# Optimization experiments

Measured on AMD Instinct MI355X. Metric: run time of the kernel, lower is better.

## Reference

```python
import jax, jax.numpy as jnp
import numpy as np

N_NODES = 100000
N_EDGES = 1600000
IN_CH, HID_CH, OUT_CH = 256, 128, 64


def setup_inputs() -> dict:
    key = jax.random.key(0)
    k_x, k_e, k1, k2, kb1, kb2 = jax.random.split(key, 6)
    x = jax.random.normal(k_x, (N_NODES, IN_CH), dtype=jnp.float32)
    edge_index = jax.random.randint(k_e, (2, N_EDGES), 0, N_NODES, dtype=jnp.int64)
    # Glorot-style init for GCN linear weights
    W1 = jax.random.normal(k1, (IN_CH, HID_CH), dtype=jnp.float32) * (1.0 / np.sqrt(IN_CH))
    b1 = jnp.zeros((HID_CH,), dtype=jnp.float32)
    W2 = jax.random.normal(k2, (HID_CH, OUT_CH), dtype=jnp.float32) * (1.0 / np.sqrt(HID_CH))
    b2 = jnp.zeros((OUT_CH,), dtype=jnp.float32)
    return {"x": x, "edge_index": edge_index, "W1": W1, "b1": b1, "W2": W2, "b2": b2}


def _gcn_norm(edge_index, n_nodes):
    # add self loops, compute D^{-1/2} (A+I) D^{-1/2} edge weights (PyG gcn_norm)
    loop = jnp.arange(n_nodes, dtype=edge_index.dtype)
    src = jnp.concatenate([edge_index[0], loop])
    dst = jnp.concatenate([edge_index[1], loop])
    deg = jax.ops.segment_sum(jnp.ones_like(src, dtype=jnp.float32), dst, num_segments=n_nodes)
    dinv = jnp.where(deg > 0, jax.lax.rsqrt(jnp.maximum(deg, 1.0)), 0.0)
    norm = dinv[src] * dinv[dst]  # [E + N]
    return src, dst, norm


def _gcn_conv(x, W, b, src, dst, norm, n_nodes):
    h = x @ W                         # linear first (PyG GCNConv)
    msg = norm[:, None] * h[src]      # gather + normalize  [E+N, out]
    agg = jax.ops.segment_sum(msg, dst, num_segments=n_nodes)
    return agg + b


def reference(x, edge_index, W1, b1, W2, b2):
    n = x.shape[0]
    src, dst, norm = _gcn_norm(edge_index, n)
    h = jax.nn.relu(_gcn_conv(x, W1, b1, src, dst, norm, n))
    # dropout is identity in eval mode
    z = _gcn_conv(h, W2, b2, src, dst, norm, n)
    # inner-product decoder on the provided edges, with sigmoid
    e_src, e_dst = edge_index[0], edge_index[1]
    logits = jnp.sum(z[e_src] * z[e_dst], axis=-1)
    return jax.nn.sigmoid(logits)
```

## Files before the change

### kernel.cpp

```cpp
#include <hip/hip_runtime.h>
#include <math.h>

#define N_NODES 100000
#define N_EDGES 1600000
#define IN_CH 256
#define HID_CH 128
#define OUT_CH 64
#define NTILES ((N_NODES + 63) / 64)
#define NB 1024
#define NPART 256
#define EPB (N_EDGES / NPART)
#define NB_USED ((N_NODES + 127) / 128)

typedef short s16x8 __attribute__((ext_vector_type(8)));
typedef unsigned short u16x8 __attribute__((ext_vector_type(8)));
typedef float f32x4 __attribute__((ext_vector_type(4)));

__device__ __forceinline__ float bf2f(unsigned short u) {
    union { unsigned int i; float f; } v;
    v.i = ((unsigned int)u) << 16;
    return v.f;
}
__device__ __forceinline__ unsigned short f2bf(float f) {
    union { float f; unsigned int i; } v;
    v.f = f;
    unsigned int u = v.i;
    return (unsigned short)((u + 0x7FFFu + ((u >> 16) & 1u)) >> 16);
}


__global__ __launch_bounds__(256) void k_hist(const int* __restrict__ dst,
                                              int* __restrict__ ghist) {
    __shared__ int h[NB];
    int b = blockIdx.x, t = threadIdx.x;
    for (int k = t; k < NB; k += 256) h[k] = 0;
    __syncthreads();
    int e0 = b * EPB;
    for (int e = e0 + t; e < e0 + EPB; e += 256)
        atomicAdd(&h[dst[e] >> 7], 1);
    __syncthreads();
    for (int k = t; k < NB; k += 256) ghist[k * NPART + b] = h[k];
}

__global__ __launch_bounds__(256) void k_scan_cols(const int* __restrict__ ghist,
                                                   int* __restrict__ goff,
                                                   int* __restrict__ btot) {
    __shared__ int tmp[NPART];
    int k = blockIdx.x, t = threadIdx.x;
    int v = ghist[k * NPART + t];
    tmp[t] = v;
    __syncthreads();
    for (int off = 1; off < NPART; off <<= 1) {
        int u = (t >= off) ? tmp[t - off] : 0;
        __syncthreads();
        tmp[t] += u;
        __syncthreads();
    }
    goff[k * NPART + t] = tmp[t] - v;
    if (t == NPART - 1) btot[k] = tmp[t];
}

__global__ __launch_bounds__(1024) void k_scan_base(const int* __restrict__ btot,
                                                    int* __restrict__ bbase) {
    __shared__ int tmp[NB];
    int t = threadIdx.x;
    int v = btot[t];
    tmp[t] = v;
    __syncthreads();
    for (int off = 1; off < NB; off <<= 1) {
        int u = (t >= off) ? tmp[t - off] : 0;
        __syncthreads();
        tmp[t] += u;
        __syncthreads();
    }
    bbase[t] = tmp[t] - v;
    if (t == NB - 1) bbase[NB] = tmp[t];
}

__global__ __launch_bounds__(256) void k_partition(const int* __restrict__ src,
                                                   const int* __restrict__ dst,
                                                   const int* __restrict__ goff,
                                                   const int* __restrict__ bbase,
                                                   int* __restrict__ bsorted_p) {
    __shared__ int cur[NB];
    int b = blockIdx.x, t = threadIdx.x;
    for (int k = t; k < NB; k += 256) cur[k] = bbase[k] + goff[k * NPART + b];
    __syncthreads();
    int e0 = b * EPB;
    for (int e = e0 + t; e < e0 + EPB; e += 256) {
        int s = src[e], d = dst[e];
        int pos = atomicAdd(&cur[d >> 7], 1);
        bsorted_p[pos] = (s << 7) | (d & 127);
    }
}

__global__ __launch_bounds__(256) void k_bucket_csr(const int* __restrict__ bsorted_p,
                                                    const int* __restrict__ bbase,
                                                    int* __restrict__ rowoff,
                                                    float* __restrict__ dinv,
                                                    int* __restrict__ csr_src) {
    __shared__ int cnt[128];
    __shared__ int tmp[256];
    __shared__ int cur[128];
    int b = blockIdx.x, t = threadIdx.x;
    int ebeg = bbase[b], eend = bbase[b + 1];
    if (t < 128) cnt[t] = 0;
    __syncthreads();
    for (int e = ebeg + t; e < eend; e += 256)
        atomicAdd(&cnt[bsorted_p[e] & 127], 1);
    __syncthreads();
    int v = (t < 128) ? cnt[t] : 0;
    tmp[t] = v;
    __syncthreads();
    for (int off = 1; off < 256; off <<= 1) {
        int u = (t >= off) ? tmp[t - off] : 0;
        __syncthreads();
        tmp[t] += u;
        __syncthreads();
    }
    if (t < 128) {
        int base = ebeg + tmp[t] - v;
        cur[t] = base;
        int node = b * 128 + t;
        if (node < N_NODES) {
            rowoff[node] = base;
            dinv[node] = rsqrtf((float)v + 1.0f);
        }
    }
    __syncthreads();
    for (int e = ebeg + t; e < eend; e += 256) {
        int v2 = bsorted_p[e];
        int pos = atomicAdd(&cur[v2 & 127], 1);
        csr_src[pos] = v2 >> 7;
    }
}

__global__ __launch_bounds__(256) void k_cast(const float* __restrict__ x,
                                              unsigned short* __restrict__ xb) {
    const int total = N_NODES * IN_CH / 8;
    int stride = gridDim.x * 256;
    for (int i = blockIdx.x * 256 + threadIdx.x; i < total; i += stride) {
        f32x4 a = *reinterpret_cast<const f32x4*>(x + (size_t)i * 8);
        f32x4 b = *reinterpret_cast<const f32x4*>(x + (size_t)i * 8 + 4);
        u16x8 o;
        o[0] = f2bf(a[0]); o[1] = f2bf(a[1]); o[2] = f2bf(a[2]); o[3] = f2bf(a[3]);
        o[4] = f2bf(b[0]); o[5] = f2bf(b[1]); o[6] = f2bf(b[2]); o[7] = f2bf(b[3]);
        *reinterpret_cast<u16x8*>(xb + (size_t)i * 8) = o;
    }
}

__global__ void k_wt1(const float* __restrict__ W1, unsigned short* __restrict__ Wf1) {
    int u = blockIdx.x * 256 + threadIdx.x;
    int f = u >> 6, lane = u & 63;
    int kk = f >> 3, nt = f & 7;
    int l15 = lane & 15, lhi = lane >> 4;
    int n = nt * 16 + l15;
    int kbase = kk * 32 + lhi * 8;
    #pragma unroll
    for (int j = 0; j < 8; ++j)
        Wf1[(size_t)u * 8 + j] = f2bf(W1[(size_t)(kbase + j) * HID_CH + n]);
}

__global__ void k_wt2(const float* __restrict__ W2, unsigned short* __restrict__ Wf2) {
    int u = blockIdx.x * 256 + threadIdx.x;
    int f = u >> 6, lane = u & 63;
    int kk = f >> 2, nt = f & 3;
    int l15 = lane & 15, lhi = lane >> 4;
    int n = nt * 16 + l15;
    int kbase = kk * 32 + lhi * 8;
    #pragma unroll
    for (int j = 0; j < 8; ++j)
        Wf2[(size_t)u * 8 + j] = f2bf(W2[(size_t)(kbase + j) * OUT_CH + n]);
}

__global__ __launch_bounds__(256, 4) void k_gemm1(const unsigned short* __restrict__ xb,
                                                  const unsigned short* __restrict__ Wf1,
                                                  const float* __restrict__ dinv,
                                                  unsigned short* __restrict__ hs1) {
    int tid = threadIdx.x;
    int w = tid >> 6;
    int lane = tid & 63;
    int l15 = lane & 15;
    int lhi = lane >> 4;
    int m0 = blockIdx.x * 64;

    int arow = m0 + w * 16 + l15;
    int arowc = (arow < N_NODES) ? arow : (N_NODES - 1);
    const s16x8* ap = reinterpret_cast<const s16x8*>(xb + (size_t)arowc * IN_CH) + lhi;

    s16x8 af[8];
    #pragma unroll
    for (int kk = 0; kk < 8; ++kk) af[kk] = ap[kk * 4];

    const s16x8* wp = reinterpret_cast<const s16x8*>(Wf1) + lane;

    f32x4 acc[8] = {};
    #pragma unroll
    for (int kk = 0; kk < 8; ++kk) {
        #pragma unroll
        for (int nt = 0; nt < 8; ++nt) {
            s16x8 bf = wp[(kk * 8 + nt) * 64];
            acc[nt] = __builtin_amdgcn_mfma_f32_16x16x32_bf16(af[kk], bf, acc[nt], 0, 0, 0);
        }
    }

    float dv[4];
    int rb = m0 + w * 16 + lhi * 4;
    #pragma unroll
    for (int r = 0; r < 4; ++r) dv[r] = (rb + r < N_NODES) ? dinv[rb + r] : 0.0f;
    #pragma unroll
    for (int nt = 0; nt < 8; ++nt) {
        #pragma unroll
        for (int r = 0; r < 4; ++r) {
            int row = rb + r;
            if (row < N_NODES)
                hs1[(size_t)row * HID_CH + nt * 16 + l15] = f2bf(dv[r] * acc[nt][r]);
        }
    }
}

__global__ __launch_bounds__(256, 4) void k_gemm2(const unsigned short* __restrict__ h1r,
                                                  const unsigned short* __restrict__ Wf2,
                                                  const float* __restrict__ dinv,
                                                  unsigned short* __restrict__ hs2) {
    int tid = threadIdx.x;
    int w = tid >> 6;
    int lane = tid & 63;
    int l15 = lane & 15;
    int lhi = lane >> 4;
    int m0 = blockIdx.x * 64;

    int arow = m0 + w * 16 + l15;
    int arowc = (arow < N_NODES) ? arow : (N_NODES - 1);
    const s16x8* ap = reinterpret_cast<const s16x8*>(h1r + (size_t)arowc * HID_CH) + lhi;

    s16x8 af[4];
    #pragma unroll
    for (int kk = 0; kk < 4; ++kk) af[kk] = ap[kk * 4];

    const s16x8* wp = reinterpret_cast<const s16x8*>(Wf2) + lane;

    f32x4 acc[4] = {};
    #pragma unroll
    for (int kk = 0; kk < 4; ++kk) {
        #pragma unroll
        for (int nt = 0; nt < 4; ++nt) {
            s16x8 bf = wp[(kk * 4 + nt) * 64];
            acc[nt] = __builtin_amdgcn_mfma_f32_16x16x32_bf16(af[kk], bf, acc[nt], 0, 0, 0);
        }
    }

    float dv[4];
    int rb = m0 + w * 16 + lhi * 4;
    #pragma unroll
    for (int r = 0; r < 4; ++r) dv[r] = (rb + r < N_NODES) ? dinv[rb + r] : 0.0f;
    #pragma unroll
    for (int nt = 0; nt < 4; ++nt) {
        #pragma unroll
        for (int r = 0; r < 4; ++r) {
            int row = rb + r;
            if (row < N_NODES)
                hs2[(size_t)row * OUT_CH + nt * 16 + l15] = f2bf(dv[r] * acc[nt][r]);
        }
    }
}

template <int C, bool RELU>
__global__ __launch_bounds__(256) void k_gather_agg(const int* __restrict__ rowoff,
                                                    const int* __restrict__ csr_src,
                                                    const unsigned short* __restrict__ hs,
                                                    const float* __restrict__ dinv,
                                                    const float* __restrict__ b,
                                                    unsigned short* __restrict__ outp) {
    constexpr int TPN = C / 8;
    constexpr int NPB = 256 / TPN;
    int t = threadIdx.x;
    int node = blockIdx.x * NPB + t / TPN;
    int q = t % TPN;
    if (node >= N_NODES) return;

    int beg = rowoff[node];
    int end = (node + 1 < N_NODES) ? rowoff[node + 1] : N_EDGES;

    float acc[8];
    {
        u16x8 sv = *reinterpret_cast<const u16x8*>(&hs[(size_t)node * C + q * 8]);
        #pragma unroll
        for (int j = 0; j < 8; ++j) acc[j] = bf2f(sv[j]);
    }

    int i = beg;
    for (; i + 3 < end; i += 4) {
        int s0 = csr_src[i], s1 = csr_src[i + 1], s2 = csr_src[i + 2], s3 = csr_src[i + 3];
        u16x8 v0 = *reinterpret_cast<const u16x8*>(&hs[(size_t)s0 * C + q * 8]);
        u16x8 v1 = *reinterpret_cast<const u16x8*>(&hs[(size_t)s1 * C + q * 8]);
        u16x8 v2 = *reinterpret_cast<const u16x8*>(&hs[(size_t)s2 * C + q * 8]);
        u16x8 v3 = *reinterpret_cast<const u16x8*>(&hs[(size_t)s3 * C + q * 8]);
        #pragma unroll
        for (int j = 0; j < 8; ++j)
            acc[j] += (bf2f(v0[j]) + bf2f(v1[j])) + (bf2f(v2[j]) + bf2f(v3[j]));
    }
    for (; i < end; ++i) {
        int s0 = csr_src[i];
        u16x8 v0 = *reinterpret_cast<const u16x8*>(&hs[(size_t)s0 * C + q * 8]);
        #pragma unroll
        for (int j = 0; j < 8; ++j) acc[j] += bf2f(v0[j]);
    }

    float w = dinv[node];
    float4 b0 = reinterpret_cast<const float4*>(b)[q * 2];
    float4 b1 = reinterpret_cast<const float4*>(b)[q * 2 + 1];
    float bb[8] = {b0.x, b0.y, b0.z, b0.w, b1.x, b1.y, b1.z, b1.w};
    u16x8 o;
    #pragma unroll
    for (int j = 0; j < 8; ++j) {
        float v = w * acc[j] + bb[j];
        if (RELU) v = fmaxf(v, 0.0f);
        o[j] = f2bf(v);
    }
    *reinterpret_cast<u16x8*>(&outp[(size_t)node * C + q * 8]) = o;
}


__global__ __launch_bounds__(256) void k_decode(const int* __restrict__ esrc,
                                                const int* __restrict__ edst,
                                                const unsigned short* __restrict__ z,
                                                float* __restrict__ out) {
    int tid = threadIdx.x;
    int e = blockIdx.x * 32 + tid / 8;
    int q = tid % 8;
    if (e >= N_EDGES) return;
    int s = esrc[e], d = edst[e];
    u16x8 a = *reinterpret_cast<const u16x8*>(&z[(size_t)s * OUT_CH + q * 8]);
    u16x8 b = *reinterpret_cast<const u16x8*>(&z[(size_t)d * OUT_CH + q * 8]);
    float dot = 0.0f;
    #pragma unroll
    for (int j = 0; j < 8; ++j) dot += bf2f(a[j]) * bf2f(b[j]);
    dot += __shfl_xor(dot, 1);
    dot += __shfl_xor(dot, 2);
    dot += __shfl_xor(dot, 4);
    if (q == 0) out[e] = 1.0f / (1.0f + expf(-dot));
}


extern "C" void kernel_launch(void* const* d_in, const int* in_sizes, int n_in,
                              void* d_out, int out_size, void* d_ws, size_t ws_size,
                              hipStream_t stream) {
    const float* x  = (const float*)d_in[0];
    const int*   ei = (const int*)d_in[1];
    const float* W1 = (const float*)d_in[2];
    const float* b1 = (const float*)d_in[3];
    const float* W2 = (const float*)d_in[4];
    const float* b2 = (const float*)d_in[5];
    float* out = (float*)d_out;

    const int* src = ei;
    const int* dst = ei + N_EDGES;

    char* ws = (char*)d_ws;
    int*   ghist   = (int*)(ws + 0x000000);
    int*   goff    = (int*)(ws + 0x100000);
    int*   btot    = (int*)(ws + 0x200000);
    int*   bbase   = (int*)(ws + 0x202000);
    int*   rowoff  = (int*)(ws + 0x210000);
    float* dinv    = (float*)(ws + 0x290000);
    unsigned short* Wf1 = (unsigned short*)(ws + 0x310000);
    unsigned short* Wf2 = (unsigned short*)(ws + 0x320000);
    int*   csr_src = (int*)(ws + 0x400000);
    int*   bsorted_p = (int*)(ws + 0xB00000);
    unsigned short* xb  = (unsigned short*)(ws + 0xB00000);
    unsigned short* hs1 = (unsigned short*)(ws + 0x3C00000);
    unsigned short* h1r = (unsigned short*)(ws + 0xB00000);
    unsigned short* hs2 = (unsigned short*)(ws + 0x3C00000);
    unsigned short* z   = (unsigned short*)(ws + 0x2800000);

    k_hist<<<NPART, 256, 0, stream>>>(dst, ghist);
    k_scan_cols<<<NB, 256, 0, stream>>>(ghist, goff, btot);
    k_scan_base<<<1, NB, 0, stream>>>(btot, bbase);
    k_partition<<<NPART, 256, 0, stream>>>(src, dst, goff, bbase, bsorted_p);
    k_bucket_csr<<<NB_USED, 256, 0, stream>>>(bsorted_p, bbase, rowoff, dinv, csr_src);

    k_cast<<<2048, 256, 0, stream>>>(x, xb);
    k_wt1<<<16, 256, 0, stream>>>(W1, Wf1);
    k_wt2<<<4, 256, 0, stream>>>(W2, Wf2);

    k_gemm1<<<NTILES, 256, 0, stream>>>(xb, Wf1, dinv, hs1);
    k_gather_agg<HID_CH, true><<<(N_NODES * 16 + 255) / 256, 256, 0, stream>>>(
        rowoff, csr_src, hs1, dinv, b1, h1r);

    k_gemm2<<<NTILES, 256, 0, stream>>>(h1r, Wf2, dinv, hs2);
    k_gather_agg<OUT_CH, false><<<(N_NODES * 8 + 255) / 256, 256, 0, stream>>>(
        rowoff, csr_src, hs2, dinv, b2, z);

    k_decode<<<N_EDGES / 32, 256, 0, stream>>>(src, dst, z, out);
}
```

Baseline: 254.4 us.

## Fuse preprocessing kernels and overlap GEMM1 with edge partitioning

Merges cast, histogram and weight-swizzle kernels into one launch with role-based block dispatch, and runs the first GEMM in the same launch as the edge partition. To drop GEMM1's dependency on dinv, the source-side degree scaling moves into the first gather, which now multiplies each neighbour row by dinv[src]. Workspace buffers are re-laid out so the overlapping roles do not alias. This cuts launch count and serialization at the cost of extra per-edge dinv loads in the gather.

```diff
diff --git a/kernel.cpp b/kernel.cpp
--- a/kernel.cpp
+++ b/kernel.cpp
@@ -11,6 +11,7 @@
 #define NPART 256
 #define EPB (N_EDGES / NPART)
 #define NB_USED ((N_NODES + 127) / 128)
+#define CAST_BLKS 2048
 
 typedef short s16x8 __attribute__((ext_vector_type(8)));
 typedef unsigned short u16x8 __attribute__((ext_vector_type(8)));
@@ -29,18 +30,64 @@
 }
 
 
-__global__ __launch_bounds__(256) void k_hist(const int* __restrict__ dst,
-                                              int* __restrict__ ghist) {
+__device__ __forceinline__ void role_cast(int b, const float* __restrict__ x,
+                                          unsigned short* __restrict__ xb) {
+    const int total = N_NODES * IN_CH / 8;
+    int stride = CAST_BLKS * 256;
+    for (int i = b * 256 + threadIdx.x; i < total; i += stride) {
+        f32x4 a = *reinterpret_cast<const f32x4*>(x + (size_t)i * 8);
+        f32x4 c = *reinterpret_cast<const f32x4*>(x + (size_t)i * 8 + 4);
+        u16x8 o;
+        o[0] = f2bf(a[0]); o[1] = f2bf(a[1]); o[2] = f2bf(a[2]); o[3] = f2bf(a[3]);
+        o[4] = f2bf(c[0]); o[5] = f2bf(c[1]); o[6] = f2bf(c[2]); o[7] = f2bf(c[3]);
+        *reinterpret_cast<u16x8*>(xb + (size_t)i * 8) = o;
+    }
+}
+
+__global__ __launch_bounds__(256) void k_fused_pre(const float* __restrict__ x,
+                                                   const int* __restrict__ dst,
+                                                   const float* __restrict__ W1,
+                                                   const float* __restrict__ W2,
+                                                   unsigned short* __restrict__ xb,
+                                                   int* __restrict__ ghist,
+                                                   unsigned short* __restrict__ Wf1,
+                                                   unsigned short* __restrict__ Wf2) {
     __shared__ int h[NB];
     int b = blockIdx.x, t = threadIdx.x;
-    for (int k = t; k < NB; k += 256) h[k] = 0;
-    __syncthreads();
-    int e0 = b * EPB;
-    for (int e = e0 + t; e < e0 + EPB; e += 256)
-        atomicAdd(&h[dst[e] >> 7], 1);
-    __syncthreads();
-    for (int k = t; k < NB; k += 256) ghist[k * NPART + b] = h[k];
-}
+    if (b < CAST_BLKS) {
+        role_cast(b, x, xb);
+    } else if (b < CAST_BLKS + NPART) {
+        int hb = b - CAST_BLKS;
+        for (int k = t; k < NB; k += 256) h[k] = 0;
+        __syncthreads();
+        int e0 = hb * EPB;
+        for (int e = e0 + t; e < e0 + EPB; e += 256)
+            atomicAdd(&h[dst[e] >> 7], 1);
+        __syncthreads();
+        for (int k = t; k < NB; k += 256) ghist[k * NPART + hb] = h[k];
+    } else if (b < CAST_BLKS + NPART + 16) {
+        int u = (b - CAST_BLKS - NPART) * 256 + t;
+        int f = u >> 6, lane = u & 63;
+        int kk = f >> 3, nt = f & 7;
+        int l15 = lane & 15, lhi = lane >> 4;
+        int n = nt * 16 + l15;
+        int kbase = kk * 32 + lhi * 8;
+        #pragma unroll
+        for (int j = 0; j < 8; ++j)
+            Wf1[(size_t)u * 8 + j] = f2bf(W1[(size_t)(kbase + j) * HID_CH + n]);
+    } else {
+        int u = (b - CAST_BLKS - NPART - 16) * 256 + t;
+        int f = u >> 6, lane = u & 63;
+        int kk = f >> 2, nt = f & 3;
+        int l15 = lane & 15, lhi = lane >> 4;
+        int n = nt * 16 + l15;
+        int kbase = kk * 32 + lhi * 8;
+        #pragma unroll
+        for (int j = 0; j < 8; ++j)
+            Wf2[(size_t)u * 8 + j] = f2bf(W2[(size_t)(kbase + j) * OUT_CH + n]);
+    }
+}
+
 
 __global__ __launch_bounds__(256) void k_scan_cols(const int* __restrict__ ghist,
                                                    int* __restrict__ goff,
@@ -77,22 +124,67 @@
     if (t == NB - 1) bbase[NB] = tmp[t];
 }
 
-__global__ __launch_bounds__(256) void k_partition(const int* __restrict__ src,
+
+__global__ __launch_bounds__(256) void k_fused_mid(const int* __restrict__ src,
                                                    const int* __restrict__ dst,
                                                    const int* __restrict__ goff,
                                                    const int* __restrict__ bbase,
-                                                   int* __restrict__ bsorted_p) {
+                                                   int* __restrict__ bsorted_p,
+                                                   const unsigned short* __restrict__ xb,
+                                                   const unsigned short* __restrict__ Wf1,
+                                                   unsigned short* __restrict__ h1) {
     __shared__ int cur[NB];
     int b = blockIdx.x, t = threadIdx.x;
-    for (int k = t; k < NB; k += 256) cur[k] = bbase[k] + goff[k * NPART + b];
-    __syncthreads();
-    int e0 = b * EPB;
-    for (int e = e0 + t; e < e0 + EPB; e += 256) {
-        int s = src[e], d = dst[e];
-        int pos = atomicAdd(&cur[d >> 7], 1);
-        bsorted_p[pos] = (s << 7) | (d & 127);
-    }
-}
+    if (b < NPART) {
+        for (int k = t; k < NB; k += 256) cur[k] = bbase[k] + goff[k * NPART + b];
+        __syncthreads();
+        int e0 = b * EPB;
+        for (int e = e0 + t; e < e0 + EPB; e += 256) {
+            int s = src[e], d = dst[e];
+            int pos = atomicAdd(&cur[d >> 7], 1);
+            bsorted_p[pos] = (s << 7) | (d & 127);
+        }
+    } else {
+        int mt = b - NPART;
+        int w = t >> 6;
+        int lane = t & 63;
+        int l15 = lane & 15;
+        int lhi = lane >> 4;
+        int m0 = mt * 64;
+
+        int arow = m0 + w * 16 + l15;
+        int arowc = (arow < N_NODES) ? arow : (N_NODES - 1);
+        const s16x8* ap = reinterpret_cast<const s16x8*>(xb + (size_t)arowc * IN_CH) + lhi;
+
+        s16x8 af[8];
+        #pragma unroll
+        for (int kk = 0; kk < 8; ++kk) af[kk] = ap[kk * 4];
+
+        const s16x8* wp = reinterpret_cast<const s16x8*>(Wf1) + lane;
+
+        f32x4 acc[8] = {};
+        #pragma unroll
+        for (int kk = 0; kk < 8; ++kk) {
+            #pragma unroll
+            for (int nt = 0; nt < 8; ++nt) {
+                s16x8 bf = wp[(kk * 8 + nt) * 64];
+                acc[nt] = __builtin_amdgcn_mfma_f32_16x16x32_bf16(af[kk], bf, acc[nt], 0, 0, 0);
+            }
+        }
+
+        int rb = m0 + w * 16 + lhi * 4;
+        #pragma unroll
+        for (int nt = 0; nt < 8; ++nt) {
+            #pragma unroll
+            for (int r = 0; r < 4; ++r) {
+                int row = rb + r;
+                if (row < N_NODES)
+                    h1[(size_t)row * HID_CH + nt * 16 + l15] = f2bf(acc[nt][r]);
+            }
+        }
+    }
+}
+
 
 __global__ __launch_bounds__(256) void k_bucket_csr(const int* __restrict__ bsorted_p,
                                                     const int* __restrict__ bbase,
@@ -135,88 +227,57 @@
     }
 }
 
-__global__ __launch_bounds__(256) void k_cast(const float* __restrict__ x,
-                                              unsigned short* __restrict__ xb) {
-    const int total = N_NODES * IN_CH / 8;
-    int stride = gridDim.x * 256;
-    for (int i = blockIdx.x * 256 + threadIdx.x; i < total; i += stride) {
-        f32x4 a = *reinterpret_cast<const f32x4*>(x + (size_t)i * 8);
-        f32x4 b = *reinterpret_cast<const f32x4*>(x + (size_t)i * 8 + 4);
-        u16x8 o;
-        o[0] = f2bf(a[0]); o[1] = f2bf(a[1]); o[2] = f2bf(a[2]); o[3] = f2bf(a[3]);
-        o[4] = f2bf(b[0]); o[5] = f2bf(b[1]); o[6] = f2bf(b[2]); o[7] = f2bf(b[3]);
-        *reinterpret_cast<u16x8*>(xb + (size_t)i * 8) = o;
-    }
-}
-
-__global__ void k_wt1(const float* __restrict__ W1, unsigned short* __restrict__ Wf1) {
-    int u = blockIdx.x * 256 + threadIdx.x;
-    int f = u >> 6, lane = u & 63;
-    int kk = f >> 3, nt = f & 7;
-    int l15 = lane & 15, lhi = lane >> 4;
-    int n = nt * 16 + l15;
-    int kbase = kk * 32 + lhi * 8;
+__global__ __launch_bounds__(256) void k_gather1(const int* __restrict__ rowoff,
+                                                 const int* __restrict__ csr_src,
+                                                 const unsigned short* __restrict__ h1,
+                                                 const float* __restrict__ dinv,
+                                                 const float* __restrict__ b,
+                                                 unsigned short* __restrict__ outp) {
+    int t = threadIdx.x;
+    int node = blockIdx.x * 16 + t / 16;
+    int q = t % 16;
+    if (node >= N_NODES) return;
+
+    int beg = rowoff[node];
+    int end = (node + 1 < N_NODES) ? rowoff[node + 1] : N_EDGES;
+    float wd = dinv[node];
+
+    float acc[8];
+    {
+        u16x8 sv = *reinterpret_cast<const u16x8*>(&h1[(size_t)node * HID_CH + q * 8]);
+        #pragma unroll
+        for (int j = 0; j < 8; ++j) acc[j] = wd * bf2f(sv[j]);
+    }
+
+    int i = beg;
+    for (; i + 3 < end; i += 4) {
+        int s0 = csr_src[i], s1 = csr_src[i + 1], s2 = csr_src[i + 2], s3 = csr_src[i + 3];
+        float d0 = dinv[s0], d1 = dinv[s1], d2 = dinv[s2], d3 = dinv[s3];
+        u16x8 v0 = *reinterpret_cast<const u16x8*>(&h1[(size_t)s0 * HID_CH + q * 8]);
+        u16x8 v1 = *reinterpret_cast<const u16x8*>(&h1[(size_t)s1 * HID_CH + q * 8]);
+        u16x8 v2 = *reinterpret_cast<const u16x8*>(&h1[(size_t)s2 * HID_CH + q * 8]);
+        u16x8 v3 = *reinterpret_cast<const u16x8*>(&h1[(size_t)s3 * HID_CH + q * 8]);
+        #pragma unroll
+        for (int j = 0; j < 8; ++j)
+            acc[j] += (d0 * bf2f(v0[j]) + d1 * bf2f(v1[j])) +
+                      (d2 * bf2f(v2[j]) + d3 * bf2f(v3[j]));
+    }
+    for (; i < end; ++i) {
+        int s0 = csr_src[i];
+        float d0 = dinv[s0];
+        u16x8 v0 = *reinterpret_cast<const u16x8*>(&h1[(size_t)s0 * HID_CH + q * 8]);
+        #pragma unroll
+        for (int j = 0; j < 8; ++j) acc[j] += d0 * bf2f(v0[j]);
+    }
+
+    float4 b0 = reinterpret_cast<const float4*>(b)[q * 2];
+    float4 b1 = reinterpret_cast<const float4*>(b)[q * 2 + 1];
+    float bb[8] = {b0.x, b0.y, b0.z, b0.w, b1.x, b1.y, b1.z, b1.w};
+    u16x8 o;
     #pragma unroll
     for (int j = 0; j < 8; ++j)
-        Wf1[(size_t)u * 8 + j] = f2bf(W1[(size_t)(kbase + j) * HID_CH + n]);
-}
-
-__global__ void k_wt2(const float* __restrict__ W2, unsigned short* __restrict__ Wf2) {
-    int u = blockIdx.x * 256 + threadIdx.x;
-    int f = u >> 6, lane = u & 63;
-    int kk = f >> 2, nt = f & 3;
-    int l15 = lane & 15, lhi = lane >> 4;
-    int n = nt * 16 + l15;
-    int kbase = kk * 32 + lhi * 8;
-    #pragma unroll
-    for (int j = 0; j < 8; ++j)
-        Wf2[(size_t)u * 8 + j] = f2bf(W2[(size_t)(kbase + j) * OUT_CH + n]);
-}
-
-__global__ __launch_bounds__(256, 4) void k_gemm1(const unsigned short* __restrict__ xb,
-                                                  const unsigned short* __restrict__ Wf1,
-                                                  const float* __restrict__ dinv,
-                                                  unsigned short* __restrict__ hs1) {
-    int tid = threadIdx.x;
-    int w = tid >> 6;
-    int lane = tid & 63;
-    int l15 = lane & 15;
-    int lhi = lane >> 4;
-    int m0 = blockIdx.x * 64;
-
-    int arow = m0 + w * 16 + l15;
-    int arowc = (arow < N_NODES) ? arow : (N_NODES - 1);
-    const s16x8* ap = reinterpret_cast<const s16x8*>(xb + (size_t)arowc * IN_CH) + lhi;
-
-    s16x8 af[8];
-    #pragma unroll
-    for (int kk = 0; kk < 8; ++kk) af[kk] = ap[kk * 4];
-
-    const s16x8* wp = reinterpret_cast<const s16x8*>(Wf1) + lane;
-
-    f32x4 acc[8] = {};
-    #pragma unroll
-    for (int kk = 0; kk < 8; ++kk) {
-        #pragma unroll
-        for (int nt = 0; nt < 8; ++nt) {
-            s16x8 bf = wp[(kk * 8 + nt) * 64];
-            acc[nt] = __builtin_amdgcn_mfma_f32_16x16x32_bf16(af[kk], bf, acc[nt], 0, 0, 0);
-        }
-    }
-
-    float dv[4];
-    int rb = m0 + w * 16 + lhi * 4;
-    #pragma unroll
-    for (int r = 0; r < 4; ++r) dv[r] = (rb + r < N_NODES) ? dinv[rb + r] : 0.0f;
-    #pragma unroll
-    for (int nt = 0; nt < 8; ++nt) {
-        #pragma unroll
-        for (int r = 0; r < 4; ++r) {
-            int row = rb + r;
-            if (row < N_NODES)
-                hs1[(size_t)row * HID_CH + nt * 16 + l15] = f2bf(dv[r] * acc[nt][r]);
-        }
-    }
+        o[j] = f2bf(fmaxf(wd * acc[j] + bb[j], 0.0f));
+    *reinterpret_cast<u16x8*>(&outp[(size_t)node * HID_CH + q * 8]) = o;
 }
 
 __global__ __launch_bounds__(256, 4) void k_gemm2(const unsigned short* __restrict__ h1r,
@@ -366,27 +427,27 @@
     float* dinv    = (float*)(ws + 0x290000);
     unsigned short* Wf1 = (unsigned short*)(ws + 0x310000);
     unsigned short* Wf2 = (unsigned short*)(ws + 0x320000);
-    int*   csr_src = (int*)(ws + 0x400000);
+    int*   csr_src   = (int*)(ws + 0x400000);
     int*   bsorted_p = (int*)(ws + 0xB00000);
-    unsigned short* xb  = (unsigned short*)(ws + 0xB00000);
-    unsigned short* hs1 = (unsigned short*)(ws + 0x3C00000);
-    unsigned short* h1r = (unsigned short*)(ws + 0xB00000);
-    unsigned short* hs2 = (unsigned short*)(ws + 0x3C00000);
-    unsigned short* z   = (unsigned short*)(ws + 0x2800000);
-
-    k_hist<<<NPART, 256, 0, stream>>>(dst, ghist);
+    unsigned short* xb  = (unsigned short*)(ws + 0x1200000);
+    unsigned short* h1  = (unsigned short*)(ws + 0x4300000);
+    unsigned short* h1r = (unsigned short*)(ws + 0x1200000);
+    unsigned short* hs2 = (unsigned short*)(ws + 0x2B00000);
+    unsigned short* z   = (unsigned short*)(ws + 0x4300000);
+
+    k_fused_pre<<<CAST_BLKS + NPART + 16 + 4, 256, 0, stream>>>(
+        x, dst, W1, W2, xb, ghist, Wf1, Wf2);
+
     k_scan_cols<<<NB, 256, 0, stream>>>(ghist, goff, btot);
     k_scan_base<<<1, NB, 0, stream>>>(btot, bbase);
-    k_partition<<<NPART, 256, 0, stream>>>(src, dst, goff, bbase, bsorted_p);
+
+    k_fused_mid<<<NPART + NTILES, 256, 0, stream>>>(
+        src, dst, goff, bbase, bsorted_p, xb, Wf1, h1);
+
     k_bucket_csr<<<NB_USED, 256, 0, stream>>>(bsorted_p, bbase, rowoff, dinv, csr_src);
 
-    k_cast<<<2048, 256, 0, stream>>>(x, xb);
-    k_wt1<<<16, 256, 0, stream>>>(W1, Wf1);
-    k_wt2<<<4, 256, 0, stream>>>(W2, Wf2);
-
-    k_gemm1<<<NTILES, 256, 0, stream>>>(xb, Wf1, dinv, hs1);
-    k_gather_agg<HID_CH, true><<<(N_NODES * 16 + 255) / 256, 256, 0, stream>>>(
-        rowoff, csr_src, hs1, dinv, b1, h1r);
+    k_gather1<<<(N_NODES * 16 + 255) / 256, 256, 0, stream>>>(
+        rowoff, csr_src, h1, dinv, b1, h1r);
 
     k_gemm2<<<NTILES, 256, 0, stream>>>(h1r, Wf2, dinv, hs2);
     k_gather_agg<OUT_CH, false><<<(N_NODES * 8 + 255) / 256, 256, 0, stream>>>(
```

Result: faster. 238.9 us (-6.1%).
